# Kernel tuning notes

Measured on AMD Instinct MI355X. Metric: run time of the kernel, lower is better.

The kernel has to match this reference:

```python
import jax, jax.numpy as jnp
import numpy as np
import math

EMBED_DIMS = 256
NUM_HEADS = 8
NUM_LEVELS = 4
NUM_POINTS = 8
SPATIAL_SHAPES = np.array([[92, 160], [46, 80], [23, 40], [12, 20]], dtype=np.int32)


def _offset_bias():
    # Faithful to reset_parameters(): per-head unit directions scaled by point index.
    thetas = np.arange(NUM_HEADS, dtype=np.float32) * (2.0 * math.pi / NUM_HEADS)
    grid = np.stack([np.cos(thetas), np.sin(thetas)], axis=-1)
    grid = grid / np.abs(grid).max(axis=-1, keepdims=True)
    grid = np.tile(grid[:, None, None, :], (1, NUM_LEVELS, NUM_POINTS, 1))
    for i in range(NUM_POINTS):
        grid[:, :, i, :] *= i + 1
    return grid.reshape(-1).astype(np.float32)


def setup_inputs() -> dict:
    key = jax.random.key(0)
    ks = jax.random.split(key, 8)
    B, Q, E = 4, 10000, EMBED_DIMS
    S = int((SPATIAL_SHAPES[:, 0] * SPATIAL_SHAPES[:, 1]).sum())
    Z = 4  # num_z_anchors; NUM_POINTS % Z == 0
    query = jax.random.normal(ks[0], (B, Q, E), dtype=jnp.float32)
    value = jax.random.normal(ks[1], (B, S, E), dtype=jnp.float32)
    reference_points = jax.random.uniform(ks[2], (B, Q, Z, 2), dtype=jnp.float32)
    # Learned params (random weights so the math is fully exercised; bias per original init).
    w_off = jax.random.normal(ks[3], (E, NUM_HEADS * NUM_LEVELS * NUM_POINTS * 2), dtype=jnp.float32) * 0.01
    b_off = jnp.asarray(_offset_bias())
    w_attn = jax.random.normal(ks[4], (E, NUM_HEADS * NUM_LEVELS * NUM_POINTS), dtype=jnp.float32) * 0.02
    b_attn = jnp.zeros((NUM_HEADS * NUM_LEVELS * NUM_POINTS,), dtype=jnp.float32)
    w_val = jax.random.normal(ks[5], (E, E), dtype=jnp.float32) * (1.0 / np.sqrt(E))
    b_val = jnp.zeros((E,), dtype=jnp.float32)
    return {
        "query": query, "value": value, "reference_points": reference_points,
        "w_off": w_off, "b_off": b_off, "w_attn": w_attn, "b_attn": b_attn,
        "w_val": w_val, "b_val": b_val,
        "spatial_shapes": jnp.asarray(SPATIAL_SHAPES),
    }


def _bilinear_sample(img, px, py):
    """grid_sample(bilinear, padding=zeros, align_corners=False).
    img: [N, H, W, D]; px, py: [N, Q, P] in pixel coords. Returns [N, Q, P, D]."""
    H, W = img.shape[1], img.shape[2]
    x0 = jnp.floor(px); y0 = jnp.floor(py)
    wx = (px - x0)[..., None]; wy = (py - y0)[..., None]
    x0i = x0.astype(jnp.int32); y0i = y0.astype(jnp.int32)
    x1i = x0i + 1; y1i = y0i + 1
    bidx = jnp.arange(img.shape[0])[:, None, None]
    def gather(yy, xx):
        m = ((yy >= 0) & (yy < H) & (xx >= 0) & (xx < W)).astype(img.dtype)[..., None]
        return img[bidx, jnp.clip(yy, 0, H - 1), jnp.clip(xx, 0, W - 1)] * m
    v00 = gather(y0i, x0i); v01 = gather(y0i, x1i)
    v10 = gather(y1i, x0i); v11 = gather(y1i, x1i)
    return (v00 * (1 - wx) + v01 * wx) * (1 - wy) + (v10 * (1 - wx) + v11 * wx) * wy


def _forward(query, value, reference_points, w_off, b_off, w_attn, b_attn, w_val, b_val, shapes_np):
    B, Q, E = query.shape
    NH, L, NP = NUM_HEADS, shapes_np.shape[0], NUM_POINTS
    D = E // NH
    v = (value @ w_val + b_val).reshape(B, -1, NH, D)  # [B, S, NH, D]
    off = (query @ w_off + b_off).reshape(B, Q, NH, L, NP, 2)
    attn = jax.nn.softmax((query @ w_attn + b_attn).reshape(B, Q, NH, L * NP), axis=-1)
    attn = attn.reshape(B, Q, NH, L, NP)
    # Normalize offsets by (W, H) per level.
    norm = jnp.asarray(np.stack([shapes_np[:, 1], shapes_np[:, 0]], axis=-1), dtype=off.dtype)  # [L,2]
    off = off / norm[None, None, None, :, None, :]
    Z = reference_points.shape[2]
    off = off.reshape(B, Q, NH, L, NP // Z, Z, 2)
    loc = reference_points[:, :, None, None, None, :, :] + off  # [B,Q,NH,L,NP/Z,Z,2]
    loc = loc.reshape(B, Q, NH, L, NP, 2)
    out = jnp.zeros((B, Q, NH, D), dtype=query.dtype)
    start = 0
    for lvl in range(L):
        hl, wl = int(shapes_np[lvl, 0]), int(shapes_np[lvl, 1])
        seg = v[:, start:start + hl * wl]
        start += hl * wl
        img = seg.reshape(B, hl, wl, NH, D).transpose(0, 3, 1, 2, 4).reshape(B * NH, hl, wl, D)
        g = loc[:, :, :, lvl].transpose(0, 2, 1, 3, 4).reshape(B * NH, Q, NP, 2)
        # align_corners=False: pixel = norm_coord * size - 0.5
        px = g[..., 0] * wl - 0.5
        py = g[..., 1] * hl - 0.5
        samp = _bilinear_sample(img, px, py)  # [B*NH, Q, NP, D]
        w = attn[:, :, :, lvl].transpose(0, 2, 1, 3).reshape(B * NH, Q, NP)
        out = out + jnp.einsum('nqpd,nqp->nqd', samp, w).reshape(B, NH, Q, D).transpose(0, 2, 1, 3)
    return out.reshape(B, Q, NH * D)


def reference(query, value, reference_points, w_off, b_off, w_attn, b_attn, w_val, b_val, spatial_shapes):
    shapes_np = np.asarray(spatial_shapes)
    return _forward(query, value, reference_points, w_off, b_off, w_attn, b_attn, w_val, b_val, shapes_np)
```

## Files before the change

kernel.cpp:

```cpp
#include <hip/hip_runtime.h>

#define BATCH    4
#define NQ       10000
#define EMB      256
#define NH       8
#define DH       32
#define NL       4
#define NP       8
#define S_TOTAL  19560
#define NROW     (BATCH * NQ)
#define VROWS    (BATCH * S_TOTAL)

typedef _Float16 half8 __attribute__((ext_vector_type(8)));
typedef _Float16 half4v __attribute__((ext_vector_type(4)));
typedef _Float16 half2v __attribute__((ext_vector_type(2)));
typedef float floatx4 __attribute__((ext_vector_type(4)));

__global__ __launch_bounds__(256) void prep_weights(
    const float* __restrict__ w_off, const float* __restrict__ w_attn,
    const float* __restrict__ w_val, _Float16* __restrict__ wT768,
    _Float16* __restrict__ wvaT) {
  const int tid = blockIdx.x * 256 + threadIdx.x;
  const int n = tid >> 8, k = tid & 255;
  const int c = k >> 3, e = k & 7;
  const int swz = ((c ^ (n & 7)) << 3) + e;
  float v;
  _Float16* dst;
  if (n < 512)      { v = w_off[(size_t)k * 512 + n];          dst = wT768 + (size_t)n * 256; }
  else if (n < 768) { v = w_attn[(size_t)k * 256 + (n - 512)]; dst = wT768 + (size_t)n * 256; }
  else              { v = w_val[(size_t)k * 256 + (n - 768)];  dst = wvaT + (size_t)(n - 768) * 256; }
  dst[swz] = (_Float16)v;
}

template <int NC, int NYS, bool SWZ>
__global__ __launch_bounds__(256, 3) void gemm6(
    const float* __restrict__ A, const _Float16* __restrict__ WTs,
    const float* __restrict__ bias0, const float* __restrict__ bias1,
    int splitc, _Float16* __restrict__ C, int M) {
  __shared__ _Float16 bsm[64 * 256];
  const int t = threadIdx.x;
  const int wave = t >> 6, lane = t & 63;
  const int l15 = lane & 15, quad = lane >> 4;
  const int m0 = blockIdx.x * 128 + wave * 32;
  const int nlo = blockIdx.y * (NC / NYS);
  const int nchunks = (NC / NYS) / 64;

  const _Float16* src = WTs + (size_t)nlo * 256;

  half8 pb[8];
  #pragma unroll
  for (int i = 0; i < 8; ++i)
    pb[i] = *(const half8*)(src + t * 8 + i * 2048);

  half8 a[2][8];
  #pragma unroll
  for (int i = 0; i < 2; ++i) {
    const float* Ar = A + (size_t)min(m0 + 16 * i + l15, M - 1) * 256 + quad * 8;
    #pragma unroll
    for (int ks = 0; ks < 8; ++ks) {
      const float4 f0 = *(const float4*)(Ar + ks * 32);
      const float4 f1 = *(const float4*)(Ar + ks * 32 + 4);
      a[i][ks][0] = (_Float16)f0.x; a[i][ks][1] = (_Float16)f0.y;
      a[i][ks][2] = (_Float16)f0.z; a[i][ks][3] = (_Float16)f0.w;
      a[i][ks][4] = (_Float16)f1.x; a[i][ks][5] = (_Float16)f1.y;
      a[i][ks][6] = (_Float16)f1.z; a[i][ks][7] = (_Float16)f1.w;
    }
  }

  #pragma unroll
  for (int i = 0; i < 8; ++i)
    *(half8*)&bsm[t * 8 + i * 2048] = pb[i];
  __syncthreads();

  for (int ch = 0; ch < nchunks; ++ch) {
    if (ch + 1 < nchunks) {
      const _Float16* s2 = src + (size_t)(ch + 1) * 64 * 256;
      #pragma unroll
      for (int i = 0; i < 8; ++i)
        pb[i] = *(const half8*)(s2 + t * 8 + i * 2048);
    }

    floatx4 acc[2][4] = {};
    #pragma unroll
    for (int ks = 0; ks < 8; ++ks) {
      half8 b[4];
      #pragma unroll
      for (int j = 0; j < 4; ++j)
        b[j] = *(const half8*)&bsm[(16 * j + l15) * 256 +
                                   ((((ks * 4 + quad) ^ (l15 & 7))) << 3)];
      if constexpr (SWZ) {
        #pragma unroll
        for (int j = 0; j < 4; ++j)
          #pragma unroll
          for (int i = 0; i < 2; ++i)
            acc[i][j] = __builtin_amdgcn_mfma_f32_16x16x32_f16(b[j], a[i][ks], acc[i][j], 0, 0, 0);
      } else {
        #pragma unroll
        for (int j = 0; j < 4; ++j)
          #pragma unroll
          for (int i = 0; i < 2; ++i)
            acc[i][j] = __builtin_amdgcn_mfma_f32_16x16x32_f16(a[i][ks], b[j], acc[i][j], 0, 0, 0);
      }
    }

    const int nc0 = nlo + ch * 64;

    if constexpr (SWZ) {
      #pragma unroll
      for (int j = 0; j < 4; ++j) {
        const int col0 = nc0 + 16 * j + quad * 4;
        const int h = col0 >> 5, c0 = col0 & 31;
        const float4 bq = *(const float4*)(bias0 + col0);
        #pragma unroll
        for (int i = 0; i < 2; ++i) {
          const int row = m0 + 16 * i + l15;
          if (row < M) {
            const int b = row / S_TOTAL;
            const int s = row - b * S_TOTAL;
            half4v pk;
            pk[0] = (_Float16)(acc[i][j][0] + bq.x);
            pk[1] = (_Float16)(acc[i][j][1] + bq.y);
            pk[2] = (_Float16)(acc[i][j][2] + bq.z);
            pk[3] = (_Float16)(acc[i][j][3] + bq.w);
            *(half4v*)(C + ((((size_t)b * NH + h) * S_TOTAL + s) * 32 + c0)) = pk;
          }
        }
      }
    } else {
      float bc[4];
      #pragma unroll
      for (int j = 0; j < 4; ++j) {
        const int col = nc0 + 16 * j + l15;
        bc[j] = (col < splitc) ? bias0[col] : bias1[col - splitc];
      }
      #pragma unroll
      for (int i = 0; i < 2; ++i) {
        #pragma unroll
        for (int r = 0; r < 4; ++r) {
          const int row = m0 + 16 * i + quad * 4 + r;
          if (row < M) {
            #pragma unroll
            for (int j = 0; j < 4; ++j)
              C[(size_t)row * NC + nc0 + 16 * j + l15] =
                  (_Float16)(acc[i][j][r] + bc[j]);
          }
        }
      }
    }

    __syncthreads();
    if (ch + 1 < nchunks) {
      #pragma unroll
      for (int i = 0; i < 8; ++i)
        *(half8*)&bsm[t * 8 + i * 2048] = pb[i];
      __syncthreads();
    }
  }
}

__global__ __launch_bounds__(256, 4) void msda_sample(
    const _Float16* __restrict__ vproj,
    const _Float16* __restrict__ fused,
    const float* __restrict__ ref,
    float* __restrict__ out) {
  const int lvl_h[NL] = {92, 46, 23, 12};
  const int lvl_w[NL] = {160, 80, 40, 20};
  const int lvl_s[NL] = {0, 14720, 18400, 19320};

  __shared__ int   addr_s[512];
  __shared__ float w2_s[1024];

  const int t   = threadIdx.x;
  const int blk = blockIdx.x;
  const int b   = blk & 3;
  const int q   = blk >> 2;
  const int row = b * NQ + q;

  const int h  = t >> 5;
  const int lp = t & 31;
  const int l  = lp >> 3;
  const int p  = lp & 7;

  const float logit = (float)fused[(size_t)row * 768 + 512 + t];
  float mxv = logit;
  #pragma unroll
  for (int m = 1; m < 32; m <<= 1) mxv = fmaxf(mxv, __shfl_xor(mxv, m));
  const float e = __expf(logit - mxv);
  float sum = e;
  #pragma unroll
  for (int m = 1; m < 32; m <<= 1) sum += __shfl_xor(sum, m);
  const float attnw = e / sum;

  const half2v o2 = *(const half2v*)(fused + (size_t)row * 768 + 2 * t);
  const float ox = (float)o2[0], oy = (float)o2[1];
  const int z = p & 3;
  const float rx = ref[((size_t)row * 4 + z) * 2 + 0];
  const float ry = ref[((size_t)row * 4 + z) * 2 + 1];
  const int Wl = lvl_w[l], Hl = lvl_h[l], st = lvl_s[l];

  const float px = fmaf(rx, (float)Wl, ox) - 0.5f;
  const float py = fmaf(ry, (float)Hl, oy) - 0.5f;
  const float x0f = floorf(px), y0f = floorf(py);
  const float wx = px - x0f, wy = py - y0f;
  const int x0 = (int)x0f, y0 = (int)y0f;
  const int x1 = x0 + 1,   y1 = y0 + 1;

  const float mx0 = (x0 >= 0 && x0 < Wl) ? 1.f : 0.f;
  const float mx1 = (x1 >= 0 && x1 < Wl) ? 1.f : 0.f;
  const float my0 = (y0 >= 0 && y0 < Hl) ? 1.f : 0.f;
  const float my1 = (y1 >= 0 && y1 < Hl) ? 1.f : 0.f;
  const int xb  = min(max(x0, -1), Wl - 1);
  const int cy0 = min(max(y0, 0), Hl - 1);
  const int cy1 = min(max(y1, 0), Hl - 1);

  const int bh   = b * NH + h;
  const int lbase = bh * S_TOTAL + st;
  const float wlc = attnw * (1.f - wx) * mx0;
  const float wrc = attnw * wx * mx1;

  addr_s[2 * t + 0] = (lbase + cy0 * Wl + xb) * 32;
  addr_s[2 * t + 1] = (lbase + cy1 * Wl + xb) * 32;
  w2_s[2 * t + 0]       = wlc * (1.f - wy) * my0;
  w2_s[2 * t + 1]       = wlc * wy * my1;
  w2_s[512 + 2 * t + 0] = wrc * (1.f - wy) * my0;
  w2_s[512 + 2 * t + 1] = wrc * wy * my1;
  __syncthreads();

  const int g  = t & 31;
  const int c  = g & 7;
  const int sd = (g >> 3) & 1;
  const int ph = g >> 4;
  const int ldoff = sd * 32 + 4 * c;
  const int wbase = sd << 9;

  half4v vt[16], vb[16];
  float wt[16], wb[16];
  #pragma unroll
  for (int i = 0; i < 16; ++i) {
    const int idx = ((h << 5) + 2 * i + ph) * 2;
    const int at = addr_s[idx], ab = addr_s[idx + 1];
    wt[i] = w2_s[wbase + idx];
    wb[i] = w2_s[wbase + idx + 1];
    vt[i] = *(const half4v*)(vproj + at + ldoff);
    vb[i] = *(const half4v*)(vproj + ab + ldoff);
  }

  float a0 = 0.f, a1 = 0.f, a2 = 0.f, a3 = 0.f;
  #pragma unroll
  for (int i = 0; i < 16; ++i) {
    a0 = fmaf(wt[i], (float)vt[i][0], a0); a1 = fmaf(wt[i], (float)vt[i][1], a1);
    a2 = fmaf(wt[i], (float)vt[i][2], a2); a3 = fmaf(wt[i], (float)vt[i][3], a3);
    a0 = fmaf(wb[i], (float)vb[i][0], a0); a1 = fmaf(wb[i], (float)vb[i][1], a1);
    a2 = fmaf(wb[i], (float)vb[i][2], a2); a3 = fmaf(wb[i], (float)vb[i][3], a3);
  }

  a0 += __shfl_xor(a0, 8);  a1 += __shfl_xor(a1, 8);
  a2 += __shfl_xor(a2, 8);  a3 += __shfl_xor(a3, 8);
  a0 += __shfl_xor(a0, 16); a1 += __shfl_xor(a1, 16);
  a2 += __shfl_xor(a2, 16); a3 += __shfl_xor(a3, 16);

  if (g < 8) {
    float4 o; o.x = a0; o.y = a1; o.z = a2; o.w = a3;
    *(float4*)(out + (size_t)row * 256 + (h << 5) + 4 * c) = o;
  }
}

extern "C" void kernel_launch(void* const* d_in, const int* in_sizes, int n_in,
                              void* d_out, int out_size, void* d_ws, size_t ws_size,
                              hipStream_t stream) {
  const float* query  = (const float*)d_in[0];
  const float* value  = (const float*)d_in[1];
  const float* refpts = (const float*)d_in[2];
  const float* w_off  = (const float*)d_in[3];
  const float* b_off  = (const float*)d_in[4];
  const float* w_attn = (const float*)d_in[5];
  const float* b_attn = (const float*)d_in[6];
  const float* w_val  = (const float*)d_in[7];
  const float* b_val  = (const float*)d_in[8];
  float* out = (float*)d_out;

  char* p = (char*)d_ws;
  p += 256;
  _Float16* vh    = (_Float16*)p;  p += (size_t)VROWS * 256 * 2;
  p += 256;
  _Float16* wT768 = (_Float16*)p;  p += (size_t)768 * 256 * 2;
  _Float16* wvaT  = (_Float16*)p;  p += (size_t)256 * 256 * 2;
  _Float16* fused_h = (_Float16*)p; p += (size_t)NROW * 768 * 2;

  prep_weights<<<1024, 256, 0, stream>>>(w_off, w_attn, w_val, wT768, wvaT);

  gemm6<256, 1, true><<<dim3((VROWS + 127) / 128, 1), 256, 0, stream>>>(
      value, wvaT, b_val, b_val, 1 << 30, vh, VROWS);
  gemm6<768, 2, false><<<dim3((NROW + 127) / 128, 2), 256, 0, stream>>>(
      query, wT768, b_off, b_attn, 512, fused_h, NROW);

  msda_sample<<<dim3(NROW), 256, 0, stream>>>(vh, fused_h, refpts, out);
}
```

Measured before the change: 398.2 us.

## Stage bilinear corner gathers through LDS with direct global-to-LDS loads

Replaces the per-thread 8-byte register gathers of value corners with 16-byte global_load_lds transfers into a per-wave LDS staging buffer, issued in four rounds. Each round waits on vmcnt and then reads half4 vectors from LDS to accumulate the weighted sum. The aim is wider, more coalesced memory transactions and lower register pressure. In exchange, the loads and the compute are serialized within each round by the explicit waits, which reduces memory-level parallelism, and the kernel uses 16KB more LDS, which may cut occupancy.

```diff
diff --git a/kernel.cpp b/kernel.cpp
--- a/kernel.cpp
+++ b/kernel.cpp
@@ -15,6 +15,9 @@
 typedef _Float16 half4v __attribute__((ext_vector_type(4)));
 typedef _Float16 half2v __attribute__((ext_vector_type(2)));
 typedef float floatx4 __attribute__((ext_vector_type(4)));
+
+#define GLOBAL_AS __attribute__((address_space(1)))
+#define LDS_AS    __attribute__((address_space(3)))
 
 __global__ __launch_bounds__(256) void prep_weights(
     const float* __restrict__ w_off, const float* __restrict__ w_attn,
@@ -167,8 +170,9 @@
   const int lvl_w[NL] = {160, 80, 40, 20};
   const int lvl_s[NL] = {0, 14720, 18400, 19320};
 
-  __shared__ int   addr_s[512];
-  __shared__ float w2_s[1024];
+  __shared__ int      addr_s[512];
+  __shared__ float    w2_s[1024];
+  __shared__ _Float16 stage[4][2048];
 
   const int t   = threadIdx.x;
   const int blk = blockIdx.x;
@@ -226,32 +230,52 @@
   w2_s[512 + 2 * t + 1] = wrc * wy * my1;
   __syncthreads();
 
+  const int wv = t >> 6;
+  const int ln = t & 63;
+  const int sub8 = ln >> 3;
+  const int chk  = ln & 7;
   const int g  = t & 31;
   const int c  = g & 7;
   const int sd = (g >> 3) & 1;
   const int ph = g >> 4;
-  const int ldoff = sd * 32 + 4 * c;
   const int wbase = sd << 9;
-
-  half4v vt[16], vb[16];
-  float wt[16], wb[16];
-  #pragma unroll
-  for (int i = 0; i < 16; ++i) {
-    const int idx = ((h << 5) + 2 * i + ph) * 2;
-    const int at = addr_s[idx], ab = addr_s[idx + 1];
-    wt[i] = w2_s[wbase + idx];
-    wb[i] = w2_s[wbase + idx + 1];
-    vt[i] = *(const half4v*)(vproj + at + ldoff);
-    vb[i] = *(const half4v*)(vproj + ab + ldoff);
-  }
+  const int h1 = h & 1;
 
   float a0 = 0.f, a1 = 0.f, a2 = 0.f, a3 = 0.f;
-  #pragma unroll
-  for (int i = 0; i < 16; ++i) {
-    a0 = fmaf(wt[i], (float)vt[i][0], a0); a1 = fmaf(wt[i], (float)vt[i][1], a1);
-    a2 = fmaf(wt[i], (float)vt[i][2], a2); a3 = fmaf(wt[i], (float)vt[i][3], a3);
-    a0 = fmaf(wb[i], (float)vb[i][0], a0); a1 = fmaf(wb[i], (float)vb[i][1], a1);
-    a2 = fmaf(wb[i], (float)vb[i][2], a2); a3 = fmaf(wb[i], (float)vb[i][3], a3);
+
+  #pragma unroll
+  for (int r = 0; r < 4; ++r) {
+    asm volatile("s_waitcnt lgkmcnt(0)" ::: "memory");
+
+    #pragma unroll
+    for (int j = 0; j < 4; ++j) {
+      const int rf  = j * 8 + sub8;
+      const int h2  = rf >> 4;
+      const int ii  = (rf >> 2) & 3;
+      const int php = (rf >> 1) & 1;
+      const int rw  = rf & 1;
+      const int lpx = 8 * r + 2 * ii + php;
+      const int aidx = (((wv * 2 + h2) << 5) + lpx) * 2 + rw;
+      const char* gp = (const char*)vproj + (ptrdiff_t)addr_s[aidx] * 2 + chk * 16;
+      __builtin_amdgcn_global_load_lds(
+          (const GLOBAL_AS void*)gp,
+          (LDS_AS void*)&stage[wv][j * 512], 16, 0, 0);
+    }
+    asm volatile("s_waitcnt vmcnt(0)" ::: "memory");
+
+    #pragma unroll
+    for (int ii = 0; ii < 4; ++ii) {
+      const int lpx = 8 * r + 2 * ii + ph;
+      const int idx = ((h << 5) + lpx) << 1;
+      const float2 wp = *(const float2*)&w2_s[wbase + idx];
+      const int rft = (h1 << 4) + (ii << 2) + (ph << 1);
+      const half4v vt = *(const half4v*)&stage[wv][rft * 64 + sd * 32 + 4 * c];
+      const half4v vb = *(const half4v*)&stage[wv][(rft + 1) * 64 + sd * 32 + 4 * c];
+      a0 = fmaf(wp.x, (float)vt[0], a0); a1 = fmaf(wp.x, (float)vt[1], a1);
+      a2 = fmaf(wp.x, (float)vt[2], a2); a3 = fmaf(wp.x, (float)vt[3], a3);
+      a0 = fmaf(wp.y, (float)vb[0], a0); a1 = fmaf(wp.y, (float)vb[1], a1);
+      a2 = fmaf(wp.y, (float)vb[2], a2); a3 = fmaf(wp.y, (float)vb[3], a3);
+    }
   }
 
   a0 += __shfl_xor(a0, 8);  a1 += __shfl_xor(a1, 8);
```

Measured after the change: 415.9 us. 1.04x slower.

## Merge the two projection GEMMs into one launch and widen sampler gathers to 16 bytes

Applied to the files above, without the earlier changes.

The value-projection and query-projection GEMMs now run in a single launch, with the block index selecting which one each block computes. This removes a kernel boundary and lets blocks of both GEMMs run together, filling the tail of the first. The sampler now has each lane fetch 8 fp16 channels (16 bytes) from one corner row instead of 4 channels from two rows, then reduces across lanes with xor shuffles at distances 4, 8 and 16. Stored addresses are offset by +64, which appears to be a trick to keep addresses unsigned when x = -1, but it adds an extra shuffle stage.

```diff
diff --git a/kernel.cpp b/kernel.cpp
--- a/kernel.cpp
+++ b/kernel.cpp
@@ -33,16 +33,16 @@
 }
 
 template <int NC, int NYS, bool SWZ>
-__global__ __launch_bounds__(256, 3) void gemm6(
+__device__ __forceinline__ void gemm_body(
     const float* __restrict__ A, const _Float16* __restrict__ WTs,
     const float* __restrict__ bias0, const float* __restrict__ bias1,
-    int splitc, _Float16* __restrict__ C, int M) {
-  __shared__ _Float16 bsm[64 * 256];
+    int splitc, _Float16* __restrict__ C, int M, int bx, int by,
+    _Float16* bsm ) {
   const int t = threadIdx.x;
   const int wave = t >> 6, lane = t & 63;
   const int l15 = lane & 15, quad = lane >> 4;
-  const int m0 = blockIdx.x * 128 + wave * 32;
-  const int nlo = blockIdx.y * (NC / NYS);
+  const int m0 = bx * 128 + wave * 32;
+  const int nlo = by * (NC / NYS);
   const int nchunks = (NC / NYS) / 64;
 
   const _Float16* src = WTs + (size_t)nlo * 256;
@@ -158,6 +158,29 @@
   }
 }
 
+#define VH_BLOCKS 612
+#define FU_BLOCKS 313
+
+__global__ __launch_bounds__(256, 3) void gemm_merged(
+    const float* __restrict__ value, const float* __restrict__ query,
+    const _Float16* __restrict__ wvaT, const _Float16* __restrict__ wT768,
+    const float* __restrict__ b_val, const float* __restrict__ b_off,
+    const float* __restrict__ b_attn,
+    _Float16* __restrict__ vh, _Float16* __restrict__ fused_h) {
+  __shared__ _Float16 bsm[64 * 256];
+  const int bid = blockIdx.x;
+  if (bid < VH_BLOCKS) {
+    gemm_body<256, 1, true>(value, wvaT, b_val, b_val, 1 << 30, vh, VROWS,
+                            bid, 0, bsm);
+  } else {
+    const int r = bid - VH_BLOCKS;
+    const int by = (r >= FU_BLOCKS) ? 1 : 0;
+    const int bx = r - by * FU_BLOCKS;
+    gemm_body<768, 2, false>(query, wT768, b_off, b_attn, 512, fused_h, NROW,
+                             bx, by, bsm);
+  }
+}
+
 __global__ __launch_bounds__(256, 4) void msda_sample(
     const _Float16* __restrict__ vproj,
     const _Float16* __restrict__ fused,
@@ -218,8 +241,8 @@
   const float wlc = attnw * (1.f - wx) * mx0;
   const float wrc = attnw * wx * mx1;
 
-  addr_s[2 * t + 0] = (lbase + cy0 * Wl + xb) * 32;
-  addr_s[2 * t + 1] = (lbase + cy1 * Wl + xb) * 32;
+  addr_s[2 * t + 0] = (lbase + cy0 * Wl + xb) * 32 + 64;
+  addr_s[2 * t + 1] = (lbase + cy1 * Wl + xb) * 32 + 64;
   w2_s[2 * t + 0]       = wlc * (1.f - wy) * my0;
   w2_s[2 * t + 1]       = wlc * wy * my1;
   w2_s[512 + 2 * t + 0] = wrc * (1.f - wy) * my0;
@@ -227,41 +250,46 @@
   __syncthreads();
 
   const int g  = t & 31;
-  const int c  = g & 7;
-  const int sd = (g >> 3) & 1;
-  const int ph = g >> 4;
-  const int ldoff = sd * 32 + 4 * c;
-  const int wbase = sd << 9;
-
-  half4v vt[16], vb[16];
-  float wt[16], wb[16];
+  const int c3 = g & 7;
+  const int rw = (g >> 3) & 1;
+  const int pg = g >> 4;
+  const uint32_t coff = (uint32_t)(c3 << 3);
+  const int wsd = (c3 >> 2) << 9;
+  const _Float16* vbase = vproj - 64;
+
+  half8 v[16];
+  float w[16];
   #pragma unroll
   for (int i = 0; i < 16; ++i) {
-    const int idx = ((h << 5) + 2 * i + ph) * 2;
-    const int at = addr_s[idx], ab = addr_s[idx + 1];
-    wt[i] = w2_s[wbase + idx];
-    wb[i] = w2_s[wbase + idx + 1];
-    vt[i] = *(const half4v*)(vproj + at + ldoff);
-    vb[i] = *(const half4v*)(vproj + ab + ldoff);
+    const int idx = (((h << 5) + 2 * i + pg) << 1) + rw;
+    w[i] = w2_s[wsd + idx];
+    v[i] = *(const half8*)(vbase + ((uint32_t)addr_s[idx] + coff));
   }
 
   float a0 = 0.f, a1 = 0.f, a2 = 0.f, a3 = 0.f;
+  float a4 = 0.f, a5 = 0.f, a6 = 0.f, a7 = 0.f;
   #pragma unroll
   for (int i = 0; i < 16; ++i) {
-    a0 = fmaf(wt[i], (float)vt[i][0], a0); a1 = fmaf(wt[i], (float)vt[i][1], a1);
-    a2 = fmaf(wt[i], (float)vt[i][2], a2); a3 = fmaf(wt[i], (float)vt[i][3], a3);
-    a0 = fmaf(wb[i], (float)vb[i][0], a0); a1 = fmaf(wb[i], (float)vb[i][1], a1);
-    a2 = fmaf(wb[i], (float)vb[i][2], a2); a3 = fmaf(wb[i], (float)vb[i][3], a3);
-  }
-
-  a0 += __shfl_xor(a0, 8);  a1 += __shfl_xor(a1, 8);
-  a2 += __shfl_xor(a2, 8);  a3 += __shfl_xor(a3, 8);
-  a0 += __shfl_xor(a0, 16); a1 += __shfl_xor(a1, 16);
-  a2 += __shfl_xor(a2, 16); a3 += __shfl_xor(a3, 16);
-
-  if (g < 8) {
-    float4 o; o.x = a0; o.y = a1; o.z = a2; o.w = a3;
-    *(float4*)(out + (size_t)row * 256 + (h << 5) + 4 * c) = o;
+    a0 = fmaf(w[i], (float)v[i][0], a0); a1 = fmaf(w[i], (float)v[i][1], a1);
+    a2 = fmaf(w[i], (float)v[i][2], a2); a3 = fmaf(w[i], (float)v[i][3], a3);
+    a4 = fmaf(w[i], (float)v[i][4], a4); a5 = fmaf(w[i], (float)v[i][5], a5);
+    a6 = fmaf(w[i], (float)v[i][6], a6); a7 = fmaf(w[i], (float)v[i][7], a7);
+  }
+
+  #pragma unroll
+  for (int m = 4; m <= 16; m <<= 1) {
+    a0 += __shfl_xor(a0, m); a1 += __shfl_xor(a1, m);
+    a2 += __shfl_xor(a2, m); a3 += __shfl_xor(a3, m);
+    a4 += __shfl_xor(a4, m); a5 += __shfl_xor(a5, m);
+    a6 += __shfl_xor(a6, m); a7 += __shfl_xor(a7, m);
+  }
+
+  if (g < 4) {
+    float* op = out + (size_t)row * 256 + (h << 5) + (g << 3);
+    float4 o0; o0.x = a0; o0.y = a1; o0.z = a2; o0.w = a3;
+    float4 o1; o1.x = a4; o1.y = a5; o1.z = a6; o1.w = a7;
+    *(float4*)op = o0;
+    *(float4*)(op + 4) = o1;
   }
 }
 
@@ -289,10 +317,8 @@
 
   prep_weights<<<1024, 256, 0, stream>>>(w_off, w_attn, w_val, wT768, wvaT);
 
-  gemm6<256, 1, true><<<dim3((VROWS + 127) / 128, 1), 256, 0, stream>>>(
-      value, wvaT, b_val, b_val, 1 << 30, vh, VROWS);
-  gemm6<768, 2, false><<<dim3((NROW + 127) / 128, 2), 256, 0, stream>>>(
-      query, wT768, b_off, b_attn, 512, fused_h, NROW);
+  gemm_merged<<<dim3(VH_BLOCKS + 2 * FU_BLOCKS), 256, 0, stream>>>(
+      value, query, wvaT, wT768, b_val, b_off, b_attn, vh, fused_h);
 
   msda_sample<<<dim3(NROW), 256, 0, stream>>>(vh, fused_h, refpts, out);
 }
```

Result: no change. 394.3 us (-1.0%).
